# Optimization experiments

Measured on AMD Instinct MI355X. Metric: run time of the kernel, lower is better.

## Reference

```python
import jax, jax.numpy as jnp
import numpy as np

B = 128          # batch of trees (same topology)
N_LEAVES = 512
N_NODES = 2 * N_LEAVES - 1   # 1023, null child slot = N_NODES
IN_DIM = 300
MEM_DIM = 300


def _build_tree():
    # complete binary tree, level order: leaves first, then parents.
    null = N_NODES
    left = [null] * N_LEAVES
    right = [null] * N_LEAVES
    prev = list(range(N_LEAVES))
    nid = N_LEAVES
    while len(prev) > 1:
        cur = []
        for k in range(0, len(prev), 2):
            left.append(prev[k]); right.append(prev[k + 1])
            cur.append(nid); nid += 1
        prev = cur
    left = np.asarray(left, np.int32)
    right = np.asarray(right, np.int32)
    leaf_mask = (left == null).astype(np.int32)
    return left, right, leaf_mask


def setup_inputs() -> dict:
    key = jax.random.key(0)
    ks = jax.random.split(key, 5)
    left, right, leaf_mask = _build_tree()
    s = 0.05  # keep gates out of saturation
    return {
        "inputs": jax.random.normal(ks[0], (B, N_NODES, IN_DIM), jnp.float32),
        "Wfioux": jax.random.normal(ks[1], (IN_DIM, 4 * MEM_DIM), jnp.float32) * s,
        "b_fioux": jax.random.normal(ks[2], (4 * MEM_DIM,), jnp.float32) * s,
        "Wiouh": jax.random.normal(ks[3], (2 * MEM_DIM, 3 * MEM_DIM), jnp.float32) * s,
        "Wfh": jax.random.normal(ks[4], (2 * MEM_DIM, 2 * MEM_DIM), jnp.float32) * s,
        "left_idx": jnp.asarray(left),
        "right_idx": jnp.asarray(right),
        "leaf_mask": jnp.asarray(leaf_mask),
    }


def _tree_lstm(inputs, Wfioux, b_fioux, Wiouh, Wfh, left_idx, right_idx, leaf_mask):
    b, n, _ = inputs.shape
    mem = Wiouh.shape[1] // 3
    # internal nodes get zero input (as in the torch code)
    x = inputs * leaf_mask.astype(inputs.dtype)[None, :, None]
    # input-dependent gates precomputed for all nodes: [n, b, 4*mem]
    fioux = jnp.einsum('bni,io->nbo', x, Wfioux) + b_fioux

    C0 = jnp.zeros((n + 1, b, mem), inputs.dtype)  # row n = null child = zeros
    H0 = jnp.zeros((n + 1, b, mem), inputs.dtype)

    def step(carry, xs):
        C, H = carry
        i, li, ri, fioux_i = xs
        ch_c = jnp.concatenate([C[li], C[ri]], axis=-1)  # [b, 2*mem]
        ch_h = jnp.concatenate([H[li], H[ri]], axis=-1)
        fx, ix, ox, ux = jnp.split(fioux_i, 4, axis=-1)
        ih, oh, uh = jnp.split(ch_h @ Wiouh, 3, axis=-1)
        i_g = jax.nn.sigmoid(ix + ih)
        o_g = jax.nn.sigmoid(ox + oh)
        u_g = jnp.tanh(ux + uh)
        f_g = jax.nn.sigmoid(jnp.tile(fx, (1, 2)) + ch_h @ Wfh)
        fc = (f_g * ch_c).reshape(b, 2, mem).sum(axis=1)
        c = i_g * u_g + fc
        h = o_g * jnp.tanh(c)
        return (C.at[li * 0 + i].set(c), H.at[i].set(h)), None

    xs = (jnp.arange(n, dtype=jnp.int32), left_idx, right_idx, fioux)
    (C, H), _ = jax.lax.scan(step, (C0, H0), xs)
    return C[n - 1], H[n - 1]  # root state (c, h), each [b, mem]


def reference(inputs, Wfioux, b_fioux, Wiouh, Wfh, left_idx, right_idx, leaf_mask):
    return _tree_lstm(inputs, Wfioux, b_fioux, Wiouh, Wfh, left_idx, right_idx, leaf_mask)
```

## Files before the change

kernel.cpp:

```cpp
#include <hip/hip_runtime.h>
#include <cstdint>

#define BATCH 128
#define NODES 1023
#define LEAVES 512
#define IN_DIM 300
#define MEM 300
#define NP 320
#define OUT_HALF (BATCH*MEM)

typedef __bf16   bf16x8 __attribute__((ext_vector_type(8)));
typedef short    s16x8  __attribute__((ext_vector_type(8)));
typedef short    s16x4  __attribute__((ext_vector_type(4)));
typedef float    f32x4  __attribute__((ext_vector_type(4)));
typedef _Float16 half_t;

__device__ __forceinline__ short f2bf(float f) {
    unsigned u = __float_as_uint(f);
    u += 0x7fff + ((u >> 16) & 1);
    return (short)(u >> 16);
}
__device__ __forceinline__ float sigf(float x)  { return 1.0f / (1.0f + __expf(-x)); }
__device__ __forceinline__ float tanhf_(float x){ return 1.0f - 2.0f / (1.0f + __expf(2.0f * x)); }

__device__ __forceinline__ f32x4 mfma16(s16x8 a, s16x8 b, f32x4 c) {
    return __builtin_amdgcn_mfma_f32_16x16x32_bf16(
        __builtin_bit_cast(bf16x8, a), __builtin_bit_cast(bf16x8, b), c, 0, 0, 0);
}

__device__ __forceinline__ void dma16(const short* src, short* ldsBase) {
    __builtin_amdgcn_global_load_lds(
        (const __attribute__((address_space(1))) unsigned int*)src,
        (__attribute__((address_space(3))) unsigned int*)ldsBase,
        16, 0, 0);
}

__global__ __launch_bounds__(256) void pack_node_w(
    const float* __restrict__ Wiouh, const float* __restrict__ Wfh, short* __restrict__ Wpk)
{
    int gid = blockIdx.x * 256 + threadIdx.x;
    if (gid >= 2000 * 64) return;
    int fb = gid >> 6, l = gid & 63;
    int kb = fb / 100, rem = fb % 100, s = rem / 20, nb = rem % 20;
    int n = nb * 16 + (l & 15);
    int kbase = kb * 32 + (l >> 4) * 8;
    short v[8];
#pragma unroll
    for (int j = 0; j < 8; ++j) {
        int kp = kbase + j;
        int side = kp >= NP;
        int kk = kp - side * NP;
        float f = 0.0f;
        if (kk < MEM && n < MEM) {
            int k = side * MEM + kk;
            f = (s < 3) ? Wiouh[(size_t)k * 900 + s * 300 + n]
                        : Wfh[(size_t)k * 600 + (s - 3) * 300 + n];
        }
        v[j] = f2bf(f);
    }
    *(s16x8*)&Wpk[(size_t)gid * 8] = *(s16x8*)v;
}

__global__ __launch_bounds__(256) void pack_leaf_w(
    const float* __restrict__ Wfioux, short* __restrict__ Wpk)
{
    int gid = blockIdx.x * 256 + threadIdx.x;
    if (gid >= 600 * 64) return;
    int fb = gid >> 6, l = gid & 63;
    int kb = fb / 60, rem = fb % 60, s = rem / 20, nb = rem % 20;
    int n = nb * 16 + (l & 15);
    int kbase = kb * 32 + (l >> 4) * 8;
    short v[8];
#pragma unroll
    for (int j = 0; j < 8; ++j) {
        int kp = kbase + j;
        float f = 0.0f;
        if (kp < IN_DIM && n < MEM)
            f = Wfioux[(size_t)kp * 1200 + (s + 1) * 300 + n];
        v[j] = f2bf(f);
    }
    *(s16x8*)&Wpk[(size_t)gid * 8] = *(s16x8*)v;
}

__global__ __launch_bounds__(256) void pack_x(
    const float* __restrict__ inputs, short* __restrict__ X)
{
    int gid = blockIdx.x * 256 + threadIdx.x;
    if (gid >= LEAVES * BATCH * (NP / 4)) return;
    int q = gid % (NP / 4);
    int rb = gid / (NP / 4);
    int b = rb % BATCH, leaf = rb / BATCH;
    short v[4] = {0, 0, 0, 0};
    if (q < IN_DIM / 4) {
        f32x4 f = *(const f32x4*)&inputs[((size_t)b * NODES + leaf) * IN_DIM + q * 4];
        v[0] = f2bf(f[0]); v[1] = f2bf(f[1]); v[2] = f2bf(f[2]); v[3] = f2bf(f[3]);
    }
    *(s16x4*)&X[(size_t)gid * 4] = *(s16x4*)v;
}

__global__ __launch_bounds__(256, 3) void leaf_mfma(
    const short* __restrict__ X, const short* __restrict__ Wpk,
    const float* __restrict__ b_fioux, half_t* __restrict__ C, short* __restrict__ H)
{
    __shared__ short Bs[4][12 * 512];
    const int t = threadIdx.x;
    const int l = t & 63, w = t >> 6;
    const int lane16 = l & 15, quad = l >> 4;

    const int bid = blockIdx.x;
    const int xcd = bid & 7, tt = bid >> 3;
    const int y = tt % 5;
    const int leaf = (tt / 5) * 8 + xcd;

    const short* Xb = X + (size_t)leaf * BATCH * NP;

    f32x4 acc[3][4][2];
#pragma unroll
    for (int s = 0; s < 3; ++s)
#pragma unroll
        for (int f = 0; f < 4; ++f)
#pragma unroll
            for (int mi = 0; mi < 2; ++mi) acc[s][f][mi] = (f32x4)(0.0f);

    s16x8 A[4][2];

#define L_STAGE(KB, BUF) do {                                                    \
    _Pragma("unroll")                                                            \
    for (int fl = w; fl < 12; fl += 4) {                                         \
        int s_ = fl >> 2, f_ = fl & 3;                                           \
        const short* src_ = Wpk +                                                \
            ((size_t)(((KB) * 3 + s_) * 20 + y * 4 + f_) * 64 + l) * 8;          \
        dma16(src_, &Bs[BUF][fl * 512]);                                         \
    } } while (0)

#define L_ALOAD(KB, SLOT) do {                                                   \
    const int koff_ = (KB) * 32 + quad * 8;                                      \
    A[SLOT][0] = *(const s16x8*)(Xb + (size_t)(w * 32 + lane16) * NP + koff_);   \
    A[SLOT][1] = *(const s16x8*)(Xb + (size_t)(w * 32 + 16 + lane16) * NP + koff_); \
} while (0)

    L_STAGE(0, 0); L_ALOAD(0, 0);
    L_STAGE(1, 1); L_ALOAD(1, 1);
    L_STAGE(2, 2); L_ALOAD(2, 2);

#define L_STEP(ST, WAITN) do {                                                   \
    asm volatile("s_waitcnt vmcnt(" #WAITN ")" ::: "memory");                    \
    __builtin_amdgcn_s_barrier();                                                \
    asm volatile("" ::: "memory");                                               \
    if ((ST) + 3 < 10) { L_STAGE((ST) + 3, ((ST) + 3) & 3);                      \
                         L_ALOAD((ST) + 3, ((ST) + 3) & 3); }                    \
    _Pragma("unroll")                                                            \
    for (int s_ = 0; s_ < 3; ++s_) {                                             \
        _Pragma("unroll")                                                        \
        for (int f_ = 0; f_ < 4; ++f_) {                                         \
            s16x8 b_ = *(const s16x8*)&Bs[(ST) & 3][(s_ * 4 + f_) * 512 + l * 8];\
            acc[s_][f_][0] = mfma16(A[(ST) & 3][0], b_, acc[s_][f_][0]);         \
            acc[s_][f_][1] = mfma16(A[(ST) & 3][1], b_, acc[s_][f_][1]);         \
        }                                                                        \
    } } while (0)

    L_STEP(0, 10); L_STEP(1, 10); L_STEP(2, 10); L_STEP(3, 10); L_STEP(4, 10);
    L_STEP(5, 10); L_STEP(6, 10); L_STEP(7, 10); L_STEP(8, 5);  L_STEP(9, 0);

#undef L_STEP
#undef L_ALOAD
#undef L_STAGE

#pragma unroll
    for (int f = 0; f < 4; ++f) {
        const int col = y * 64 + f * 16 + lane16;
        const bool valid = col < MEM;
        float bi = 0, bo = 0, bu = 0;
        if (valid) { bi = b_fioux[300 + col]; bo = b_fioux[600 + col]; bu = b_fioux[900 + col]; }
#pragma unroll
        for (int mi = 0; mi < 2; ++mi)
#pragma unroll
            for (int r = 0; r < 4; ++r) {
                int b = w * 32 + mi * 16 + quad * 4 + r;
                size_t hIdx = ((size_t)leaf * BATCH + b) * NP + col;
                if (valid) {
                    float ig = sigf(acc[0][f][mi][r] + bi);
                    float og = sigf(acc[1][f][mi][r] + bo);
                    float ug = tanhf_(acc[2][f][mi][r] + bu);
                    float c = ig * ug;
                    float h = og * tanhf_(c);
                    C[((size_t)leaf * BATCH + b) * MEM + col] = (half_t)c;
                    H[hIdx] = f2bf(h);
                } else {
                    H[hIdx] = 0;
                }
            }
    }
}

__global__ __launch_bounds__(256, 3) void node_mfma(
    const short* __restrict__ Wpk, const float* __restrict__ b_fioux,
    const int* __restrict__ left_idx, const int* __restrict__ right_idx,
    half_t* __restrict__ C, short* __restrict__ H,
    int level_start, int level_size, float* __restrict__ out)
{
    __shared__ short Bs[4][12 * 512];
    const int t = threadIdx.x;
    const int l = t & 63, w = t >> 6;
    const int lane16 = l & 15, quad = l >> 4;

    const int bid = blockIdx.x;
    int nidx, y;
    if ((level_size & 7) == 0) {
        const int xcd = bid & 7, tt = bid >> 3;
        y = tt % 10;
        nidx = (tt / 10) * 8 + xcd;
    } else {
        nidx = bid % level_size;
        y = bid / level_size;
    }
    const int node = level_start + nidx;

    const int li = left_idx[node], ri = right_idx[node];
    const short* HL = H + (size_t)li * BATCH * NP;
    const short* HR = H + (size_t)ri * BATCH * NP;

    f32x4 acc[5][2][2];
#pragma unroll
    for (int s = 0; s < 5; ++s)
#pragma unroll
        for (int f = 0; f < 2; ++f)
#pragma unroll
            for (int mi = 0; mi < 2; ++mi) acc[s][f][mi] = (f32x4)(0.0f);

    s16x8 A[4][2];

#define N_STAGE(KB, BUF) do {                                                    \
    _Pragma("unroll")                                                            \
    for (int fl = w; fl < 12; fl += 4) {                                         \
        int rfl_ = (fl < 10) ? fl : fl - 10;               \
        int s_ = rfl_ >> 1, f_ = rfl_ & 1;                                       \
        const short* src_ = Wpk +                                                \
            ((size_t)(((KB) * 5 + s_) * 20 + y * 2 + f_) * 64 + l) * 8;          \
        dma16(src_, &Bs[BUF][fl * 512]);                                         \
    } } while (0)

#define N_ALOAD(KB, SLOT) do {                                                   \
    const short* Hb_ = (((KB) >= 10) ? HR : HL) +                                \
                       ((KB) - (((KB) >= 10) ? 10 : 0)) * 32 + quad * 8;         \
    A[SLOT][0] = *(const s16x8*)(Hb_ + (size_t)(w * 32 + lane16) * NP);          \
    A[SLOT][1] = *(const s16x8*)(Hb_ + (size_t)(w * 32 + 16 + lane16) * NP);     \
} while (0)

    N_STAGE(0, 0); N_ALOAD(0, 0);
    N_STAGE(1, 1); N_ALOAD(1, 1);
    N_STAGE(2, 2); N_ALOAD(2, 2);

#define N_STEP(ST, WAITN) do {                                                   \
    asm volatile("s_waitcnt vmcnt(" #WAITN ")" ::: "memory");                    \
    __builtin_amdgcn_s_barrier();                                                \
    asm volatile("" ::: "memory");                                               \
    if ((ST) + 3 < 20) { N_STAGE((ST) + 3, ((ST) + 3) & 3);                      \
                         N_ALOAD((ST) + 3, ((ST) + 3) & 3); }                    \
    _Pragma("unroll")                                                            \
    for (int s_ = 0; s_ < 5; ++s_) {                                             \
        _Pragma("unroll")                                                        \
        for (int f_ = 0; f_ < 2; ++f_) {                                         \
            s16x8 b_ = *(const s16x8*)&Bs[(ST) & 3][(s_ * 2 + f_) * 512 + l * 8];\
            acc[s_][f_][0] = mfma16(A[(ST) & 3][0], b_, acc[s_][f_][0]);         \
            acc[s_][f_][1] = mfma16(A[(ST) & 3][1], b_, acc[s_][f_][1]);         \
        }                                                                        \
    } } while (0)

    N_STEP(0, 10);  N_STEP(1, 10);  N_STEP(2, 10);  N_STEP(3, 10);  N_STEP(4, 10);
    N_STEP(5, 10);  N_STEP(6, 10);  N_STEP(7, 10);  N_STEP(8, 10);  N_STEP(9, 10);
    N_STEP(10, 10); N_STEP(11, 10); N_STEP(12, 10); N_STEP(13, 10); N_STEP(14, 10);
    N_STEP(15, 10); N_STEP(16, 10); N_STEP(17, 10); N_STEP(18, 5);  N_STEP(19, 0);

#undef N_STEP
#undef N_ALOAD
#undef N_STAGE

#pragma unroll
    for (int f = 0; f < 2; ++f) {
        const int col = y * 32 + f * 16 + lane16;
        const bool valid = col < MEM;
        float bff = 0, bi = 0, bo = 0, bu = 0;
        if (valid) {
            bff = b_fioux[col]; bi = b_fioux[300 + col];
            bo = b_fioux[600 + col]; bu = b_fioux[900 + col];
        }
#pragma unroll
        for (int mi = 0; mi < 2; ++mi)
#pragma unroll
            for (int r = 0; r < 4; ++r) {
                int row = w * 32 + mi * 16 + quad * 4 + r;
                size_t hIdx = ((size_t)node * BATCH + row) * NP + col;
                if (valid) {
                    float cl = (float)C[((size_t)li * BATCH + row) * MEM + col];
                    float cr = (float)C[((size_t)ri * BATCH + row) * MEM + col];
                    float ig = sigf(acc[0][f][mi][r] + bi);
                    float og = sigf(acc[1][f][mi][r] + bo);
                    float ug = tanhf_(acc[2][f][mi][r] + bu);
                    float fl = sigf(acc[3][f][mi][r] + bff);
                    float fr = sigf(acc[4][f][mi][r] + bff);
                    float c = ig * ug + fl * cl + fr * cr;
                    float h = og * tanhf_(c);
                    C[((size_t)node * BATCH + row) * MEM + col] = (half_t)c;
                    H[hIdx] = f2bf(h);
                    if (out) {
                        out[row * MEM + col] = c;
                        out[OUT_HALF + row * MEM + col] = h;
                    }
                } else {
                    H[hIdx] = 0;
                }
            }
    }
}

extern "C" void kernel_launch(void* const* d_in, const int* in_sizes, int n_in,
                              void* d_out, int out_size, void* d_ws, size_t ws_size,
                              hipStream_t stream) {
    const float* inputs  = (const float*)d_in[0];
    const float* Wfioux  = (const float*)d_in[1];
    const float* b_fioux = (const float*)d_in[2];
    const float* Wiouh   = (const float*)d_in[3];
    const float* Wfh     = (const float*)d_in[4];
    const int*   left_idx  = (const int*)d_in[5];
    const int*   right_idx = (const int*)d_in[6];

    half_t* C   = (half_t*)d_ws;
    short*  H   = (short*)(C + (size_t)NODES * BATCH * MEM);
    short* WpkN = H + (size_t)NODES * BATCH * NP;
    short* WpkL = WpkN + (size_t)2000 * 512;
    short* X    = WpkL + (size_t)600 * 512;
    float* out  = (float*)d_out;

    pack_x<<<(LEAVES * BATCH * (NP / 4) + 255) / 256, 256, 0, stream>>>(inputs, X);
    pack_leaf_w<<<150, 256, 0, stream>>>(Wfioux, WpkL);
    pack_node_w<<<500, 256, 0, stream>>>(Wiouh, Wfh, WpkN);

    leaf_mfma<<<LEAVES * 5, 256, 0, stream>>>(X, WpkL, b_fioux, C, H);

    static const int starts[9] = {512, 768, 896, 960, 992, 1008, 1016, 1020, 1022};
    static const int sizes [9] = {256, 128,  64,  32,  16,    8,    4,    2,    1};
    for (int lvl = 0; lvl < 9; ++lvl) {
        bool root = (lvl == 8);
        node_mfma<<<sizes[lvl] * 10, 256, 0, stream>>>(
            WpkN, b_fioux, left_idx, right_idx, C, H, starts[lvl], sizes[lvl],
            root ? out : nullptr);
    }
}
```

Before: 627.8 us.

## Add deeper-pipelined K64-staged node kernel for small upper tree levels

Adds a node kernel that streams weights in 64-wide K stages through a 4-buffer shared-memory ring with 3-stage lookahead and prefetches H operands into registers. It is used for tree levels 3 and up, where only a few blocks run and per-block latency dominates. The large early levels keep the original kernel. The deeper pipeline costs more shared memory and registers, limiting occupancy to about two blocks per CU.

```diff
diff --git a/kernel.cpp b/kernel.cpp
--- a/kernel.cpp
+++ b/kernel.cpp
@@ -314,6 +314,134 @@
     }
 }
 
+__global__ __launch_bounds__(256, 2) void node_k64(
+    const short* __restrict__ Wpk, const float* __restrict__ b_fioux,
+    const int* __restrict__ left_idx, const int* __restrict__ right_idx,
+    half_t* __restrict__ C, short* __restrict__ H,
+    int level_start, int level_size, float* __restrict__ out)
+{
+    __shared__ short Bs[4][20 * 512];
+    const int t = threadIdx.x;
+    const int l = t & 63, w = t >> 6;
+    const int lane16 = l & 15, quad = l >> 4;
+
+    const int bid = blockIdx.x;
+    int nidx, y;
+    if ((level_size & 7) == 0) {
+        const int xcd = bid & 7, tt = bid >> 3;
+        y = tt % 10;
+        nidx = (tt / 10) * 8 + xcd;
+    } else {
+        nidx = bid % level_size;
+        y = bid / level_size;
+    }
+    const int node = level_start + nidx;
+
+    const int li = left_idx[node], ri = right_idx[node];
+    const short* HL = H + (size_t)li * BATCH * NP;
+    const short* HR = H + (size_t)ri * BATCH * NP;
+
+    f32x4 acc[5][2][2];
+#pragma unroll
+    for (int s = 0; s < 5; ++s)
+#pragma unroll
+        for (int f = 0; f < 2; ++f)
+#pragma unroll
+            for (int mi = 0; mi < 2; ++mi) acc[s][f][mi] = (f32x4)(0.0f);
+
+    s16x8 A[4][2][2];
+
+#define K_STAGE(ST, BUF) do {                                                    \
+    _Pragma("unroll")                                                            \
+    for (int fl = w; fl < 20; fl += 4) {                   \
+        int ksub_ = fl / 10, rem_ = fl - ksub_ * 10;                             \
+        int s_ = rem_ >> 1, f_ = rem_ & 1;                                       \
+        int kb32_ = (ST) * 2 + ksub_;                                            \
+        const short* src_ = Wpk +                                                \
+            ((size_t)((kb32_ * 5 + s_) * 20 + y * 2 + f_) * 64 + l) * 8;         \
+        dma16(src_, &Bs[BUF][fl * 512]);                                         \
+    } } while (0)
+
+#define K_ALOAD(ST, SLOT) do {                                                   \
+    const int side_ = (ST) >= 5;                                                 \
+    const short* Hb_ = (side_ ? HR : HL) + ((ST) - side_ * 5) * 64 + quad * 8;   \
+    _Pragma("unroll")                                                            \
+    for (int ksub_ = 0; ksub_ < 2; ++ksub_) {                                    \
+        A[SLOT][ksub_][0] = *(const s16x8*)(Hb_ +                                \
+            (size_t)(w * 32 + lane16) * NP + ksub_ * 32);                        \
+        A[SLOT][ksub_][1] = *(const s16x8*)(Hb_ +                                \
+            (size_t)(w * 32 + 16 + lane16) * NP + ksub_ * 32);                   \
+    } } while (0)
+
+    K_STAGE(0, 0); K_ALOAD(0, 0);
+    K_STAGE(1, 1); K_ALOAD(1, 1);
+    K_STAGE(2, 2); K_ALOAD(2, 2);
+
+#define K_STEP(ST, WAITN) do {                                                   \
+    asm volatile("s_waitcnt vmcnt(" #WAITN ")" ::: "memory");                    \
+    __builtin_amdgcn_s_barrier();                                                \
+    asm volatile("" ::: "memory");                                               \
+    if ((ST) + 3 < 10) { K_STAGE((ST) + 3, ((ST) + 3) & 3);                      \
+                         K_ALOAD((ST) + 3, ((ST) + 3) & 3); }                    \
+    _Pragma("unroll")                                                            \
+    for (int ks_ = 0; ks_ < 2; ++ks_) {                                          \
+        _Pragma("unroll")                                                        \
+        for (int s_ = 0; s_ < 5; ++s_) {                                         \
+            _Pragma("unroll")                                                    \
+            for (int f_ = 0; f_ < 2; ++f_) {                                     \
+                s16x8 b_ = *(const s16x8*)                                       \
+                    &Bs[(ST) & 3][(ks_ * 10 + s_ * 2 + f_) * 512 + l * 8];       \
+                acc[s_][f_][0] = mfma16(A[(ST) & 3][ks_][0], b_, acc[s_][f_][0]);\
+                acc[s_][f_][1] = mfma16(A[(ST) & 3][ks_][1], b_, acc[s_][f_][1]);\
+            }                                                                    \
+        }                                                                        \
+    } } while (0)
+
+    K_STEP(0, 18); K_STEP(1, 18); K_STEP(2, 18); K_STEP(3, 18); K_STEP(4, 18);
+    K_STEP(5, 18); K_STEP(6, 18); K_STEP(7, 18); K_STEP(8, 9);  K_STEP(9, 0);
+
+#undef K_STEP
+#undef K_ALOAD
+#undef K_STAGE
+
+#pragma unroll
+    for (int f = 0; f < 2; ++f) {
+        const int col = y * 32 + f * 16 + lane16;
+        const bool valid = col < MEM;
+        float bff = 0, bi = 0, bo = 0, bu = 0;
+        if (valid) {
+            bff = b_fioux[col]; bi = b_fioux[300 + col];
+            bo = b_fioux[600 + col]; bu = b_fioux[900 + col];
+        }
+#pragma unroll
+        for (int mi = 0; mi < 2; ++mi)
+#pragma unroll
+            for (int r = 0; r < 4; ++r) {
+                int row = w * 32 + mi * 16 + quad * 4 + r;
+                size_t hIdx = ((size_t)node * BATCH + row) * NP + col;
+                if (valid) {
+                    float cl = (float)C[((size_t)li * BATCH + row) * MEM + col];
+                    float cr = (float)C[((size_t)ri * BATCH + row) * MEM + col];
+                    float ig = sigf(acc[0][f][mi][r] + bi);
+                    float og = sigf(acc[1][f][mi][r] + bo);
+                    float ug = tanhf_(acc[2][f][mi][r] + bu);
+                    float fl = sigf(acc[3][f][mi][r] + bff);
+                    float fr = sigf(acc[4][f][mi][r] + bff);
+                    float c = ig * ug + fl * cl + fr * cr;
+                    float h = og * tanhf_(c);
+                    C[((size_t)node * BATCH + row) * MEM + col] = (half_t)c;
+                    H[hIdx] = f2bf(h);
+                    if (out) {
+                        out[row * MEM + col] = c;
+                        out[OUT_HALF + row * MEM + col] = h;
+                    }
+                } else {
+                    H[hIdx] = 0;
+                }
+            }
+    }
+}
+
 extern "C" void kernel_launch(void* const* d_in, const int* in_sizes, int n_in,
                               void* d_out, int out_size, void* d_ws, size_t ws_size,
                               hipStream_t stream) {
@@ -342,8 +470,14 @@
     static const int sizes [9] = {256, 128,  64,  32,  16,    8,    4,    2,    1};
     for (int lvl = 0; lvl < 9; ++lvl) {
         bool root = (lvl == 8);
-        node_mfma<<<sizes[lvl] * 10, 256, 0, stream>>>(
-            WpkN, b_fioux, left_idx, right_idx, C, H, starts[lvl], sizes[lvl],
-            root ? out : nullptr);
-    }
-}
+        if (lvl < 3) {
+            node_mfma<<<sizes[lvl] * 10, 256, 0, stream>>>(
+                WpkN, b_fioux, left_idx, right_idx, C, H, starts[lvl], sizes[lvl],
+                nullptr);
+        } else {
+            node_k64<<<sizes[lvl] * 10, 256, 0, stream>>>(
+                WpkN, b_fioux, left_idx, right_idx, C, H, starts[lvl], sizes[lvl],
+                root ? out : nullptr);
+        }
+    }
+}
```

Result: no change. 628.0 us (+0.0%).
